# Optimization experiments

Hardware: AMD Instinct MI355X
Metric: run time of the kernel (lower is better)

## Reference

```python
import jax, jax.numpy as jnp
import numpy as np

D_MODEL = 1024
NUM_HEADS = 16
D_K = D_MODEL // NUM_HEADS
B, S = 2, 2048


def setup_inputs() -> dict:
    key = jax.random.key(0)
    ks = jax.random.split(key, 6)
    scale = 1.0 / np.sqrt(D_MODEL)
    x = jax.random.normal(ks[0], (B, S, D_MODEL), dtype=jnp.float32)
    # causal mask: 1 where masked (future positions), per masked_fill(mask == 1, -inf)
    mask = jnp.triu(jnp.ones((S, S), dtype=jnp.int32), k=1)
    Wq = jax.random.normal(ks[1], (D_MODEL, D_MODEL), dtype=jnp.float32) * scale
    Wk = jax.random.normal(ks[2], (D_MODEL, D_MODEL), dtype=jnp.float32) * scale
    Wv = jax.random.normal(ks[3], (D_MODEL, D_MODEL), dtype=jnp.float32) * scale
    Wo = jax.random.normal(ks[4], (D_MODEL, D_MODEL), dtype=jnp.float32) * scale
    zeros = jnp.zeros((D_MODEL,), dtype=jnp.float32)
    return {"x": x, "mask": mask, "Wq": Wq, "bq": zeros, "Wk": Wk, "bk": zeros,
            "Wv": Wv, "bv": zeros, "Wo": Wo, "bo": zeros}


def reference(x, mask, Wq, bq, Wk, bk, Wv, bv, Wo, bo):
    b, s, d = x.shape
    # linear projections (torch nn.Linear: x @ W^T + b; here W stored as [in, out])
    Q = x @ Wq + bq
    K = x @ Wk + bk
    V = x @ Wv + bv
    # split heads -> (b, h, s, d_k)
    def split(t):
        return t.reshape(b, s, NUM_HEADS, D_K).transpose(0, 2, 1, 3)
    Q, K, V = split(Q), split(K), split(V)
    scale = 1.0 / jnp.sqrt(jnp.float32(D_K))
    scores = jnp.einsum("bhqd,bhkd->bhqk", Q, K) * scale  # (b,h,s,s)
    scores = jnp.where(mask[None, None, :, :] == 1, -jnp.inf, scores)
    attn = jax.nn.softmax(scores, axis=-1)
    out = jnp.einsum("bhqk,bhkd->bhqd", attn, V)
    out = out.transpose(0, 2, 1, 3).reshape(b, s, d)  # concat heads
    return out @ Wo + bo
```

## Files before the change

### kernel.cpp

```cpp
#include <hip/hip_runtime.h>
#include <hip/hip_bf16.h>
#include <cstdint>
#include <cmath>

#define DM 1024
#define NH 16
#define DK 64
#define NB 2
#define SS 2048
#define MM (NB*SS)

typedef unsigned short u16;
typedef uint32_t u32;
typedef __attribute__((ext_vector_type(4))) float f32x4;
typedef __attribute__((ext_vector_type(8))) short s16x8;
typedef __attribute__((ext_vector_type(4))) short s16x4;
typedef __attribute__((ext_vector_type(2))) uint32_t u32x2;

__device__ __forceinline__ u16 f2bf(float f) {
    __hip_bfloat16 h = __float2bfloat16(f);
    return __builtin_bit_cast(u16, h);
}
__device__ __forceinline__ float bf2f(u16 u) {
    u32 x = (u32)u << 16;
    return __builtin_bit_cast(float, x);
}

__device__ __forceinline__ u32 cvtpk(float a, float b) {
    u32 r;
    asm("v_cvt_pk_bf16_f32 %0, %1, %2" : "=v"(r) : "v"(a), "v"(b));
    return r;
}

__device__ __forceinline__ void gload_lds16(void* lds, const void* g) {
    __builtin_amdgcn_global_load_lds(
        (const __attribute__((address_space(1))) uint32_t*)g,
        (__attribute__((address_space(3))) uint32_t*)lds, 16, 0, 0);
}

__device__ __forceinline__ int swz(int row, int cb) {
    return row * 128 + ((((cb) >> 4) ^ (row & 7)) << 4) + ((cb) & 15);
}

__global__ void mha_cast_x(const float* __restrict__ x, u16* __restrict__ xb) {
    int i = (blockIdx.x * 256 + threadIdx.x) * 4;
    float4 v = *reinterpret_cast<const float4*>(x + i);
    ushort4 o;
    o.x = f2bf(v.x); o.y = f2bf(v.y); o.z = f2bf(v.z); o.w = f2bf(v.w);
    *reinterpret_cast<ushort4*>(xb + i) = o;
}

__global__ void mha_transW(const float* __restrict__ W0, const float* __restrict__ W1,
                           const float* __restrict__ W2, const float* __restrict__ W3,
                           u16* __restrict__ WtBase) {
    __shared__ float t[32][33];
    const int mat = blockIdx.z;
    const float* W = (mat == 0) ? W0 : (mat == 1) ? W1 : (mat == 2) ? W2 : W3;
    u16* Wt = WtBase + (size_t)mat * DM * DM;
    const int c0 = blockIdx.x * 32, r0 = blockIdx.y * 32;
    const int tx = threadIdx.x, ty = threadIdx.y;
#pragma unroll
    for (int i = ty; i < 32; i += 8)
        t[i][tx] = W[(size_t)(r0 + i) * DM + c0 + tx];
    __syncthreads();
#pragma unroll
    for (int i = ty; i < 32; i += 8)
        Wt[(size_t)(c0 + i) * DM + r0 + tx] = f2bf(t[tx][i]);
}

template<int MODE>
__device__ __forceinline__ void gemm_core(const u16* __restrict__ A, const u16* __restrict__ Bt,
                                          const float* __restrict__ bias, float scale,
                                          void* __restrict__ Cout) {
    __shared__ u16 As[128][64];
    __shared__ u16 Bs[128][64];
    const int tid = threadIdx.x;
    const int wave = tid >> 6, lane = tid & 63;
    const int lr = lane & 15, kg = lane >> 4;
    const int m0 = blockIdx.x * 128;
    const int n0 = blockIdx.y * 128;
    const int wr = wave >> 1, wc = wave & 1;
    f32x4 acc[4][4] = {};

    for (int k0 = 0; k0 < DM; k0 += 64) {
        __syncthreads();
#pragma unroll
        for (int i = 0; i < 4; ++i) {
            const int o   = ((wave * 4 + i) * 64 + lane) * 16;
            const int row = o >> 7;
            const int kb  = o & 127;
            gload_lds16((char*)As + o, A  + (size_t)(m0 + row) * DM + k0 + (kb >> 1));
            gload_lds16((char*)Bs + o, Bt + (size_t)(n0 + row) * DM + k0 + (kb >> 1));
        }
        __syncthreads();
#pragma unroll
        for (int kk = 0; kk < 64; kk += 32) {
            s16x8 a[4], b[4];
#pragma unroll
            for (int m = 0; m < 4; ++m)
                a[m] = *reinterpret_cast<const s16x8*>(&As[wr * 64 + m * 16 + lr][kk + kg * 8]);
#pragma unroll
            for (int n = 0; n < 4; ++n)
                b[n] = *reinterpret_cast<const s16x8*>(&Bs[wc * 64 + n * 16 + lr][kk + kg * 8]);
#pragma unroll
            for (int m = 0; m < 4; ++m)
#pragma unroll
                for (int n = 0; n < 4; ++n)
                    acc[m][n] = __builtin_amdgcn_mfma_f32_16x16x32_bf16(a[m], b[n], acc[m][n], 0, 0, 0);
        }
    }
#pragma unroll
    for (int m = 0; m < 4; ++m)
#pragma unroll
        for (int n = 0; n < 4; ++n) {
            const int col = n0 + wc * 64 + n * 16 + lr;
            const float bv = bias[col];
#pragma unroll
            for (int j = 0; j < 4; ++j) {
                const int row = m0 + wr * 64 + m * 16 + kg * 4 + j;
                const float v = (acc[m][n][j] + bv) * scale;
                if (MODE == 0) {
                    const int bb = row >> 11, s = row & (SS - 1);
                    const int h  = col >> 6,  d = col & (DK - 1);
                    ((u16*)Cout)[(((size_t)(bb * NH + h) * SS + s) * DK) + d] = f2bf(v);
                } else {
                    ((float*)Cout)[(size_t)row * DM + col] = v;
                }
            }
        }
}

__global__ __launch_bounds__(256, 2) void mha_gemm_qkv(const u16* __restrict__ xb, const u16* __restrict__ Wt,
                                                       const float* __restrict__ bq, const float* __restrict__ bk,
                                                       const float* __restrict__ bv, u16* __restrict__ qkv) {
    const int z = blockIdx.z;
    const float* bias = (z == 0) ? bq : (z == 1) ? bk : bv;
    const float scale = (z == 0) ? 0.125f * 1.44269504088896f : 1.0f;
    gemm_core<0>(xb, Wt + (size_t)z * DM * DM, bias, scale, qkv + (size_t)z * MM * DM);
}

__global__ __launch_bounds__(256, 2) void mha_gemm_out(const u16* __restrict__ AO, const u16* __restrict__ WoT,
                                                       const float* __restrict__ bo, float* __restrict__ out) {
    gemm_core<1>(AO, WoT, bo, 1.0f, out);
}

__device__ const unsigned char JQT[48] = {
    15,31,30,31, 14,29,30,28,29, 13,27,28,26,27, 12,25,26,24,25,
    11,23,24,22,23, 10,21,22,20,21, 9,19,20,18,19, 8,17,18,16,17,
    7,16, 6,5,4,3,2,1,0};
__device__ const unsigned char JKS[48] = {
    0,0,15,16, 0,0,0,14,15, 0,0,0,13,14, 0,0,0,12,13,
    0,0,0,11,12, 0,0,0,10,11, 0,0,0,9,10, 0,0,0,8,9,
    0,0, 0,0,0,0,0,0,0};
__device__ const unsigned char JKL[48] = {
    16,16,16,16, 15,15,15,15,15, 14,14,14,14,14, 13,13,13,13,13,
    12,12,12,12,12, 11,11,11,11,11, 10,10,10,10,10, 9,9,9,9,9,
    8,8, 7,6,5,4,3,2,1};
__device__ const unsigned char JSL[48] = {
    255,30,29,31, 255,26,28,25,27, 255,22,24,21,23, 255,18,20,17,19,
    255,14,16,13,15, 255,10,12,9,11, 255,6,8,5,7, 255,2,4,1,3,
    255,0, 255,255,255,255,255,255,255};

__device__ __forceinline__ void load_kv(s16x8 kr[2], s16x4 va[2], s16x4 vb[2],
                                        const u16* __restrict__ Kh, const u16* __restrict__ Vh,
                                        int kb, int tid) {
#pragma unroll
    for (int i = 0; i < 2; ++i) {
        const int s = tid + i * 256;
        kr[i] = *reinterpret_cast<const s16x8*>(Kh + (size_t)(kb + (s >> 3)) * DK + (s & 7) * 8);
        const int vrp = s >> 4, vc = (s & 15) * 4;
        va[i] = *reinterpret_cast<const s16x4*>(Vh + (size_t)(kb + 2 * vrp) * DK + vc);
        vb[i] = *reinterpret_cast<const s16x4*>(Vh + (size_t)(kb + 2 * vrp + 1) * DK + vc);
    }
}

__device__ __forceinline__ void store_kv(char* ksb, char* vtb, int tid,
                                         const s16x8 kr[2], const s16x4 va[2], const s16x4 vb[2]) {
#pragma unroll
    for (int i = 0; i < 2; ++i) {
        const int s = tid + i * 256;
        *reinterpret_cast<s16x8*>(ksb + swz(s >> 3, (s & 7) * 16)) = kr[i];
        const int vrp = s >> 4, vc = (s & 15) * 4;
#pragma unroll
        for (int j = 0; j < 4; ++j) {
            u32 pv = (u32)(u16)va[i][j] | ((u32)(u16)vb[i][j] << 16);
            *reinterpret_cast<u32*>(vtb + swz(vc + j, vrp * 4)) = pv;
        }
    }
}

__global__ __launch_bounds__(256, 4) void mha_attn(const u16* __restrict__ Qb, const u16* __restrict__ Kb,
                                                   const u16* __restrict__ Vb, u16* __restrict__ AO,
                                                   u16* __restrict__ Opart, float* __restrict__ lpart) {
    __shared__ __align__(16) char lds[24576];

    const int bid = blockIdx.x;
    const int bh  = bid & 31;
    const int job = bid >> 5;
    const int qt   = JQT[job];
    const int kst  = JKS[job];
    const int klen = JKL[job];
    const int slot = JSL[job];
    const int qb = qt * 64;

    const int tid = threadIdx.x, w = tid >> 6, lane = tid & 63;
    const int lr = lane & 15, kg = lane >> 4;

    const u16* Qh = Qb + (size_t)bh * SS * DK;
    const u16* Kh = Kb + (size_t)bh * SS * DK;
    const u16* Vh = Vb + (size_t)bh * SS * DK;
    const int bb = bh >> 4, hh = bh & (NH - 1);
    char* psb = lds + 16384 + w * 2048;

    const int qrow = qb + w * 16 + lr;
    const s16x8 qf0 = *reinterpret_cast<const s16x8*>(Qh + (size_t)qrow * DK + kg * 8);
    const s16x8 qf1 = *reinterpret_cast<const s16x8*>(Qh + (size_t)qrow * DK + 32 + kg * 8);
    f32x4 accO[4] = {};
    float lp = 0.f;

    const int kend = kst + klen;
    s16x8 kr[2]; s16x4 va[2], vb[2];
    load_kv(kr, va, vb, Kh, Vh, kst * 64, tid);
    store_kv(lds, lds + 8192, tid, kr, va, vb);
    __syncthreads();

    for (int t = kst; t < kend; ++t) {
        const int kb = t * 64;
        if (t + 1 < kend) load_kv(kr, va, vb, Kh, Vh, kb + 64, tid);

        f32x4 sc[4];
#pragma unroll
        for (int f = 0; f < 4; ++f) {
            s16x8 kf0 = *reinterpret_cast<const s16x8*>(lds + swz(f * 16 + lr, kg * 16));
            s16x8 kf1 = *reinterpret_cast<const s16x8*>(lds + swz(f * 16 + lr, 64 + kg * 16));
            f32x4 s = {};
            s = __builtin_amdgcn_mfma_f32_16x16x32_bf16(kf0, qf0, s, 0, 0, 0);
            s = __builtin_amdgcn_mfma_f32_16x16x32_bf16(kf1, qf1, s, 0, 0, 0);
            sc[f] = s;
        }
#pragma unroll
        for (int f = 0; f < 4; ++f)
#pragma unroll
            for (int j = 0; j < 4; ++j)
                sc[f][j] = exp2f(sc[f][j]);
        if (t == qt) {
            const int qloc = w * 16 + lr;
#pragma unroll
            for (int f = 0; f < 4; ++f) {
                const int kc = f * 16 + kg * 4;
#pragma unroll
                for (int j = 0; j < 4; ++j)
                    if (kc + j > qloc) sc[f][j] = 0.f;
            }
        }
        float fs0 = 0.f, fs1 = 0.f;
#pragma unroll
        for (int f = 0; f < 4; ++f) {
            u32x2 pp;
            pp[0] = cvtpk(sc[f][0], sc[f][1]);
            pp[1] = cvtpk(sc[f][2], sc[f][3]);
            *reinterpret_cast<u32x2*>(psb + swz(lr, f * 32 + kg * 8)) = pp;
            const float s01 = sc[f][0] + sc[f][1], s23 = sc[f][2] + sc[f][3];
            if (f & 1) fs1 += s01 + s23; else fs0 += s01 + s23;
        }
        lp += fs0 + fs1;

        const s16x8 pf0 = *reinterpret_cast<const s16x8*>(psb + swz(lr, kg * 16));
        const s16x8 pf1 = *reinterpret_cast<const s16x8*>(psb + swz(lr, 64 + kg * 16));
#pragma unroll
        for (int db = 0; db < 4; ++db) {
            s16x8 vf0 = *reinterpret_cast<const s16x8*>(lds + 8192 + swz(db * 16 + lr, kg * 16));
            s16x8 vf1 = *reinterpret_cast<const s16x8*>(lds + 8192 + swz(db * 16 + lr, 64 + kg * 16));
            accO[db] = __builtin_amdgcn_mfma_f32_16x16x32_bf16(pf0, vf0, accO[db], 0, 0, 0);
            accO[db] = __builtin_amdgcn_mfma_f32_16x16x32_bf16(pf1, vf1, accO[db], 0, 0, 0);
        }
        __syncthreads();
        if (t + 1 < kend)
            store_kv(lds, lds + 8192, tid, kr, va, vb);
        __syncthreads();
    }

    lp += __shfl_xor(lp, 16, 64);
    lp += __shfl_xor(lp, 32, 64);

    if (slot == 255) {
        float inv[4];
#pragma unroll
        for (int j = 0; j < 4; ++j)
            inv[j] = 1.0f / __shfl(lp, kg * 4 + j, 64);
#pragma unroll
        for (int db = 0; db < 4; ++db) {
            const int d = db * 16 + lr;
#pragma unroll
            for (int j = 0; j < 4; ++j) {
                const int s = qb + w * 16 + kg * 4 + j;
                AO[((size_t)(bb * SS + s)) * DM + hh * DK + d] = f2bf(accO[db][j] * inv[j]);
            }
        }
    } else {
        const int idx = bh * 32 + slot;
        u16* Od = Opart + (size_t)idx * 4096;
#pragma unroll
        for (int db = 0; db < 4; ++db) {
            const int d = db * 16 + lr;
#pragma unroll
            for (int j = 0; j < 4; ++j)
                Od[(w * 16 + kg * 4 + j) * 64 + d] = f2bf(accO[db][j]);
        }
        if (lane < 16)
            lpart[idx * 64 + w * 16 + lane] = lp;
    }
}

__global__ __launch_bounds__(256) void mha_combine(const u16* __restrict__ Opart,
                                                   const float* __restrict__ lpart,
                                                   u16* __restrict__ AO) {
    const int blk = blockIdx.x;
    const int bh = blk & 31, q = blk >> 5;
    const int qt = 16 + q;
    const int t = threadIdx.x;
    const int row = t >> 2, c0 = (t & 3) * 16;
    const int idx0 = bh * 32 + q * 2;
    const u16* O0 = Opart + (size_t)idx0 * 4096 + row * 64 + c0;
    const u16* O1 = O0 + 4096;
    const float l = lpart[idx0 * 64 + row] + lpart[(idx0 + 1) * 64 + row];
    const float inv = 1.0f / l;
    const int bb = bh >> 4, hh = bh & (NH - 1);
    const int s = qt * 64 + row;
    u16* dst = AO + ((size_t)(bb * SS + s)) * DM + hh * DK + c0;
#pragma unroll
    for (int h = 0; h < 2; ++h) {
        s16x8 a = *reinterpret_cast<const s16x8*>(O0 + h * 8);
        s16x8 b = *reinterpret_cast<const s16x8*>(O1 + h * 8);
        u16* ap = (u16*)&a; u16* bp = (u16*)&b;
        u16 ov[8];
#pragma unroll
        for (int i = 0; i < 8; ++i)
            ov[i] = f2bf((bf2f(ap[i]) + bf2f(bp[i])) * inv);
        *reinterpret_cast<ushort4*>(dst + h * 8) = *reinterpret_cast<ushort4*>(&ov[0]);
        *reinterpret_cast<ushort4*>(dst + h * 8 + 4) = *reinterpret_cast<ushort4*>(&ov[4]);
    }
}

extern "C" void kernel_launch(void* const* d_in, const int* in_sizes, int n_in,
                              void* d_out, int out_size, void* d_ws, size_t ws_size,
                              hipStream_t stream) {
    const float* x  = (const float*)d_in[0];
    const float* Wq = (const float*)d_in[2];
    const float* bq = (const float*)d_in[3];
    const float* Wk = (const float*)d_in[4];
    const float* bk = (const float*)d_in[5];
    const float* Wv = (const float*)d_in[6];
    const float* bv = (const float*)d_in[7];
    const float* Wo = (const float*)d_in[8];
    const float* bo = (const float*)d_in[9];
    float* out = (float*)d_out;

    char* ws = (char*)d_ws;
    u16* xb  = (u16*)(ws);
    u16* Wt  = (u16*)(ws + ((size_t)8  << 20));
    u16* qkv = (u16*)(ws + ((size_t)16 << 20));
    u16* AO  = (u16*)(ws + ((size_t)40 << 20));
    u16*   Opart = (u16*)(ws);
    float* lpart = (float*)(ws + ((size_t)8 << 20));

    mha_cast_x<<<dim3(4096), dim3(256), 0, stream>>>(x, xb);
    mha_transW<<<dim3(32, 32, 4), dim3(32, 8), 0, stream>>>(Wq, Wk, Wv, Wo, Wt);
    mha_gemm_qkv<<<dim3(32, 8, 3), dim3(256), 0, stream>>>(xb, Wt, bq, bk, bv, qkv);
    mha_attn<<<dim3(1536), dim3(256), 0, stream>>>(qkv, qkv + (size_t)4194304, qkv + (size_t)8388608,
                                                   AO, Opart, lpart);
    mha_combine<<<dim3(512), dim3(256), 0, stream>>>(Opart, lpart, AO);
    mha_gemm_out<<<dim3(32, 8), dim3(256), 0, stream>>>(AO, Wt + (size_t)3 * DM * DM, bo, out);
}
```

Baseline: 118.8 us.

## Pre-swizzle K/V tiles in QKV GEMM and double-buffer direct global-to-LDS loads

The QKV projection now writes K and a transposed V directly into per-64-row tiles in the same swizzled byte layout the attention kernel expects. The attention kernel can then stream whole tiles with global-to-LDS 16-byte loads into a double buffer, replacing the register round-trip and per-element V transpose, and it needs one barrier per iteration instead of two. LDS use rises from 24KB to 40KB per block, which may limit occupancy at 4 blocks per CU. exp2f is also switched to the hardware exp2 builtin.

```diff
diff --git a/kernel.cpp b/kernel.cpp
--- a/kernel.cpp
+++ b/kernel.cpp
@@ -14,7 +14,6 @@
 typedef uint32_t u32;
 typedef __attribute__((ext_vector_type(4))) float f32x4;
 typedef __attribute__((ext_vector_type(8))) short s16x8;
-typedef __attribute__((ext_vector_type(4))) short s16x4;
 typedef __attribute__((ext_vector_type(2))) uint32_t u32x2;
 
 __device__ __forceinline__ u16 f2bf(float f) {
@@ -119,12 +118,21 @@
             for (int j = 0; j < 4; ++j) {
                 const int row = m0 + wr * 64 + m * 16 + kg * 4 + j;
                 const float v = (acc[m][n][j] + bv) * scale;
-                if (MODE == 0) {
+                if (MODE == 1) {
+                    ((float*)Cout)[(size_t)row * DM + col] = v;
+                } else {
                     const int bb = row >> 11, s = row & (SS - 1);
                     const int h  = col >> 6,  d = col & (DK - 1);
-                    ((u16*)Cout)[(((size_t)(bb * NH + h) * SS + s) * DK) + d] = f2bf(v);
-                } else {
-                    ((float*)Cout)[(size_t)row * DM + col] = v;
+                    if (MODE == 0) {
+                        ((u16*)Cout)[(((size_t)(bb * NH + h) * SS + s) * DK) + d] = f2bf(v);
+                    } else {
+                        const int kt = s >> 6, r = s & 63;
+                        const size_t tb = ((size_t)(bb * NH + h) * 32 + kt) * 4096;
+                        int bo;
+                        if (MODE == 2) bo = swz(r, d * 2);
+                        else { const int cb = (r >> 1) * 4 + (r & 1) * 2; bo = swz(d, cb); }
+                        ((u16*)Cout)[tb + (bo >> 1)] = f2bf(v);
+                    }
                 }
             }
         }
@@ -134,9 +142,9 @@
                                                        const float* __restrict__ bq, const float* __restrict__ bk,
                                                        const float* __restrict__ bv, u16* __restrict__ qkv) {
     const int z = blockIdx.z;
-    const float* bias = (z == 0) ? bq : (z == 1) ? bk : bv;
-    const float scale = (z == 0) ? 0.125f * 1.44269504088896f : 1.0f;
-    gemm_core<0>(xb, Wt + (size_t)z * DM * DM, bias, scale, qkv + (size_t)z * MM * DM);
+    if (z == 0)      gemm_core<0>(xb, Wt,                        bq, 0.125f * 1.44269504088896f, qkv);
+    else if (z == 1) gemm_core<2>(xb, Wt + (size_t)DM * DM,      bk, 1.0f, qkv + (size_t)MM * DM);
+    else             gemm_core<3>(xb, Wt + (size_t)2 * DM * DM,  bv, 1.0f, qkv + (size_t)2 * MM * DM);
 }
 
 __global__ __launch_bounds__(256, 2) void mha_gemm_out(const u16* __restrict__ AO, const u16* __restrict__ WoT,
@@ -161,38 +169,10 @@
     255,14,16,13,15, 255,10,12,9,11, 255,6,8,5,7, 255,2,4,1,3,
     255,0, 255,255,255,255,255,255,255};
 
-__device__ __forceinline__ void load_kv(s16x8 kr[2], s16x4 va[2], s16x4 vb[2],
-                                        const u16* __restrict__ Kh, const u16* __restrict__ Vh,
-                                        int kb, int tid) {
-#pragma unroll
-    for (int i = 0; i < 2; ++i) {
-        const int s = tid + i * 256;
-        kr[i] = *reinterpret_cast<const s16x8*>(Kh + (size_t)(kb + (s >> 3)) * DK + (s & 7) * 8);
-        const int vrp = s >> 4, vc = (s & 15) * 4;
-        va[i] = *reinterpret_cast<const s16x4*>(Vh + (size_t)(kb + 2 * vrp) * DK + vc);
-        vb[i] = *reinterpret_cast<const s16x4*>(Vh + (size_t)(kb + 2 * vrp + 1) * DK + vc);
-    }
-}
-
-__device__ __forceinline__ void store_kv(char* ksb, char* vtb, int tid,
-                                         const s16x8 kr[2], const s16x4 va[2], const s16x4 vb[2]) {
-#pragma unroll
-    for (int i = 0; i < 2; ++i) {
-        const int s = tid + i * 256;
-        *reinterpret_cast<s16x8*>(ksb + swz(s >> 3, (s & 7) * 16)) = kr[i];
-        const int vrp = s >> 4, vc = (s & 15) * 4;
-#pragma unroll
-        for (int j = 0; j < 4; ++j) {
-            u32 pv = (u32)(u16)va[i][j] | ((u32)(u16)vb[i][j] << 16);
-            *reinterpret_cast<u32*>(vtb + swz(vc + j, vrp * 4)) = pv;
-        }
-    }
-}
-
-__global__ __launch_bounds__(256, 4) void mha_attn(const u16* __restrict__ Qb, const u16* __restrict__ Kb,
-                                                   const u16* __restrict__ Vb, u16* __restrict__ AO,
+__global__ __launch_bounds__(256, 4) void mha_attn(const u16* __restrict__ Qb, const u16* __restrict__ Kswz,
+                                                   const u16* __restrict__ Vtswz, u16* __restrict__ AO,
                                                    u16* __restrict__ Opart, float* __restrict__ lpart) {
-    __shared__ __align__(16) char lds[24576];
+    __shared__ __align__(16) char lds[40960];
 
     const int bid = blockIdx.x;
     const int bh  = bid & 31;
@@ -207,10 +187,11 @@
     const int lr = lane & 15, kg = lane >> 4;
 
     const u16* Qh = Qb + (size_t)bh * SS * DK;
-    const u16* Kh = Kb + (size_t)bh * SS * DK;
-    const u16* Vh = Vb + (size_t)bh * SS * DK;
+    const char* Ktiles = (const char*)(Kswz  + (size_t)bh * 32 * 4096);
+    const char* Vtiles = (const char*)(Vtswz + (size_t)bh * 32 * 4096);
     const int bb = bh >> 4, hh = bh & (NH - 1);
-    char* psb = lds + 16384 + w * 2048;
+    char* psb = lds + 32768 + w * 2048;
+    const int o = tid * 16;
 
     const int qrow = qb + w * 16 + lr;
     const s16x8 qf0 = *reinterpret_cast<const s16x8*>(Qh + (size_t)qrow * DK + kg * 8);
@@ -219,20 +200,37 @@
     float lp = 0.f;
 
     const int kend = kst + klen;
-    s16x8 kr[2]; s16x4 va[2], vb[2];
-    load_kv(kr, va, vb, Kh, Vh, kst * 64, tid);
-    store_kv(lds, lds + 8192, tid, kr, va, vb);
-    __syncthreads();
+    {
+        const char* Kt = Ktiles + kst * 8192;
+        const char* Vt = Vtiles + kst * 8192;
+        gload_lds16(lds + o,                 Kt + o);
+        gload_lds16(lds + o + 4096,          Kt + o + 4096);
+        gload_lds16(lds + 16384 + o,         Vt + o);
+        gload_lds16(lds + 16384 + o + 4096,  Vt + o + 4096);
+    }
 
     for (int t = kst; t < kend; ++t) {
-        const int kb = t * 64;
-        if (t + 1 < kend) load_kv(kr, va, vb, Kh, Vh, kb + 64, tid);
+        const int buf = (t - kst) & 1;
+        asm volatile("s_waitcnt vmcnt(0)" ::: "memory");
+        __syncthreads();
+        if (t + 1 < kend) {
+            const char* Kt = Ktiles + (t + 1) * 8192;
+            const char* Vt = Vtiles + (t + 1) * 8192;
+            char* kb2 = lds + (buf ^ 1) * 8192;
+            char* vb2 = lds + 16384 + (buf ^ 1) * 8192;
+            gload_lds16(kb2 + o,        Kt + o);
+            gload_lds16(kb2 + o + 4096, Kt + o + 4096);
+            gload_lds16(vb2 + o,        Vt + o);
+            gload_lds16(vb2 + o + 4096, Vt + o + 4096);
+        }
+        const char* ksb = lds + buf * 8192;
+        const char* vtb = lds + 16384 + buf * 8192;
 
         f32x4 sc[4];
 #pragma unroll
         for (int f = 0; f < 4; ++f) {
-            s16x8 kf0 = *reinterpret_cast<const s16x8*>(lds + swz(f * 16 + lr, kg * 16));
-            s16x8 kf1 = *reinterpret_cast<const s16x8*>(lds + swz(f * 16 + lr, 64 + kg * 16));
+            s16x8 kf0 = *reinterpret_cast<const s16x8*>(ksb + swz(f * 16 + lr, kg * 16));
+            s16x8 kf1 = *reinterpret_cast<const s16x8*>(ksb + swz(f * 16 + lr, 64 + kg * 16));
             f32x4 s = {};
             s = __builtin_amdgcn_mfma_f32_16x16x32_bf16(kf0, qf0, s, 0, 0, 0);
             s = __builtin_amdgcn_mfma_f32_16x16x32_bf16(kf1, qf1, s, 0, 0, 0);
@@ -242,7 +240,7 @@
         for (int f = 0; f < 4; ++f)
 #pragma unroll
             for (int j = 0; j < 4; ++j)
-                sc[f][j] = exp2f(sc[f][j]);
+                sc[f][j] = __builtin_amdgcn_exp2f(sc[f][j]);
         if (t == qt) {
             const int qloc = w * 16 + lr;
 #pragma unroll
@@ -269,15 +267,11 @@
         const s16x8 pf1 = *reinterpret_cast<const s16x8*>(psb + swz(lr, 64 + kg * 16));
 #pragma unroll
         for (int db = 0; db < 4; ++db) {
-            s16x8 vf0 = *reinterpret_cast<const s16x8*>(lds + 8192 + swz(db * 16 + lr, kg * 16));
-            s16x8 vf1 = *reinterpret_cast<const s16x8*>(lds + 8192 + swz(db * 16 + lr, 64 + kg * 16));
+            s16x8 vf0 = *reinterpret_cast<const s16x8*>(vtb + swz(db * 16 + lr, kg * 16));
+            s16x8 vf1 = *reinterpret_cast<const s16x8*>(vtb + swz(db * 16 + lr, 64 + kg * 16));
             accO[db] = __builtin_amdgcn_mfma_f32_16x16x32_bf16(pf0, vf0, accO[db], 0, 0, 0);
             accO[db] = __builtin_amdgcn_mfma_f32_16x16x32_bf16(pf1, vf1, accO[db], 0, 0, 0);
         }
-        __syncthreads();
-        if (t + 1 < kend)
-            store_kv(lds, lds + 8192, tid, kr, va, vb);
-        __syncthreads();
     }
 
     lp += __shfl_xor(lp, 16, 64);
```

After: 139.7 us. +17.5%, slower.
